# Kernel tuning notes

Hardware: AMD Instinct MI355X
Metric: run time of the kernel (lower is better)

## Reference

```python
import jax, jax.numpy as jnp
import numpy as np

C = 256        # in_channels
HEADS = 8
HD = 64        # dim_heads
INNER = HEADS * HD   # 512
G = 32         # norm_groups
FF = 4 * INNER # 2048
EPS = 1e-5


def setup_inputs() -> dict:
    key = jax.random.key(0)
    ks = jax.random.split(key, 12)
    r = lambda k, shp: jax.random.normal(k, shp, jnp.float32) * 0.02
    return {
        "x": jax.random.normal(ks[0], (1, C, 16, 16, 16), jnp.float32),
        "gn_g": jnp.ones((C,), jnp.float32),
        "gn_b": jnp.zeros((C,), jnp.float32),
        "w_in": r(ks[1], (INNER, C)),   # Conv3d 1x1x1 as (out,in) matrix
        "b_in": jnp.zeros((INNER,), jnp.float32),
        "wq": r(ks[2], (INNER, INNER)),
        "wk": r(ks[3], (INNER, INNER)),
        "wv": r(ks[4], (INNER, INNER)),
        "ln1_g": jnp.ones((INNER,), jnp.float32),
        "ln1_b": jnp.zeros((INNER,), jnp.float32),
        "ff_w1": r(ks[5], (FF, INNER)),
        "ff_b1": jnp.zeros((FF,), jnp.float32),
        "ff_w2": r(ks[6], (INNER, FF)),
        "ff_b2": jnp.zeros((INNER,), jnp.float32),
        "ln2_g": jnp.ones((INNER,), jnp.float32),
        "ln2_b": jnp.zeros((INNER,), jnp.float32),
        "w_out": r(ks[7], (C, INNER)),  # Conv3d 1x1x1 back to C
        "b_out": jnp.zeros((C,), jnp.float32),
    }


def _group_norm(x, g, b):
    # x: (B,C,D,H,W), G groups, normalize over (C//G, D, H, W)
    B, Cc, D, H, W = x.shape
    xr = x.reshape(B, G, Cc // G, D, H, W)
    mu = jnp.mean(xr, axis=(2, 3, 4, 5), keepdims=True)
    var = jnp.var(xr, axis=(2, 3, 4, 5), keepdims=True)
    xr = (xr - mu) * jax.lax.rsqrt(var + EPS)
    xn = xr.reshape(B, Cc, D, H, W)
    return xn * g[None, :, None, None, None] + b[None, :, None, None, None]


def _layer_norm(x, g, b):
    mu = jnp.mean(x, axis=-1, keepdims=True)
    var = jnp.var(x, axis=-1, keepdims=True)
    return (x - mu) * jax.lax.rsqrt(var + EPS) * g + b


def reference(x, gn_g, gn_b, w_in, b_in, wq, wk, wv, ln1_g, ln1_b,
              ff_w1, ff_b1, ff_w2, ff_b2, ln2_g, ln2_b, w_out, b_out):
    B, Cc, D, H, W = x.shape
    x_in = x
    # GroupNorm + proj_in (1x1x1 conv == channel matmul)
    h = _group_norm(x, gn_g, gn_b)
    t = jnp.einsum('bcdhw,oc->bodhw', h, w_in) + b_in[None, :, None, None, None]
    N = D * H * W
    t = t.reshape(B, INNER, N).transpose(0, 2, 1)  # (B, N, INNER)

    # self-attention (manual einsum softmax einsum)
    q = (t @ wq.T).reshape(B, N, HEADS, HD)
    k = (t @ wk.T).reshape(B, N, HEADS, HD)
    v = (t @ wv.T).reshape(B, N, HEADS, HD)
    scale = HD ** (-0.5)
    scores = jnp.einsum('bihd,bjhd->bhij', q, k) * scale  # (B,H,N,N)
    attn = jax.nn.softmax(scores, axis=-1)
    o = jnp.einsum('bhij,bjhd->bihd', attn, v).reshape(B, N, INNER)
    # out_proj is Identity (q_dim == inner_dim), dropout=0
    t = _layer_norm(o + t, ln1_g, ln1_b)

    # FeedForward: Linear -> GELU (erf) -> Linear
    ff = jax.nn.gelu(t @ ff_w1.T + ff_b1, approximate=False) @ ff_w2.T + ff_b2
    t = _layer_norm(ff + t, ln2_g, ln2_b)

    # proj_out + residual
    y = t.transpose(0, 2, 1).reshape(B, INNER, D, H, W)
    out = jnp.einsum('bidhw,oi->bodhw', y, w_out) + b_out[None, :, None, None, None]
    return out + x_in
```

## Files before the change

### kernel.cpp

```cpp
#include <hip/hip_runtime.h>
#include <hip/hip_bf16.h>

typedef unsigned short u16;
typedef __attribute__((ext_vector_type(8))) short short8;
typedef __attribute__((ext_vector_type(4))) float floatx4;

#define LOG2E 1.44269504088896f
#define CEXP (0.125f * LOG2E)

static __device__ __forceinline__ u16 f2b(float f) {
  union { float f; unsigned u; } v; v.f = f;
  unsigned r = v.u + 0x7fffu + ((v.u >> 16) & 1u);
  return (u16)(r >> 16);
}
static __device__ __forceinline__ float b2f(u16 b) {
  union { float f; unsigned u; } v; v.u = ((unsigned)b) << 16;
  return v.f;
}
static __device__ __forceinline__ void async16(const u16* g, u16* l) {
  __builtin_amdgcn_global_load_lds(
      (const __attribute__((address_space(1))) unsigned int*)g,
      (__attribute__((address_space(3))) unsigned int*)l, 16, 0, 0);
}
static __device__ __forceinline__ float fexp2(float x) {
  return __builtin_amdgcn_exp2f(x);
}

__global__ __launch_bounds__(256) void f2b_all(
    const float* __restrict__ s0, const float* __restrict__ s1, const float* __restrict__ s2,
    const float* __restrict__ s3, const float* __restrict__ s4, const float* __restrict__ s5,
    const float* __restrict__ s6, const float* __restrict__ x,
    u16* __restrict__ d_win, u16* __restrict__ d_qkv, u16* __restrict__ d_f1,
    u16* __restrict__ d_f2, u16* __restrict__ d_wout, float2* __restrict__ cstats) {
  if (blockIdx.x >= 12288) {
    int c = blockIdx.x - 12288;
    const float4* p4 = (const float4*)(x + (size_t)c * 4096);
    float s = 0.f, ss = 0.f;
#pragma unroll
    for (int j = 0; j < 4; j++) {
      float4 v = p4[j * 256 + threadIdx.x];
      s += v.x + v.y + v.z + v.w;
      ss += v.x * v.x + v.y * v.y + v.z * v.z + v.w * v.w;
    }
    for (int m = 1; m < 64; m <<= 1) { s += __shfl_xor(s, m); ss += __shfl_xor(ss, m); }
    __shared__ float sb[8];
    int w = threadIdx.x >> 6;
    if ((threadIdx.x & 63) == 0) { sb[w * 2] = s; sb[w * 2 + 1] = ss; }
    __syncthreads();
    if (threadIdx.x == 0)
      cstats[c] = float2{sb[0] + sb[2] + sb[4] + sb[6], sb[1] + sb[3] + sb[5] + sb[7]};
    return;
  }
  int i = blockIdx.x * 256 + threadIdx.x;
  if (i < 131072) { d_win[i] = f2b(s0[i]); return; }
  i -= 131072;
  if (i < 262144) { d_qkv[i] = f2b(s1[i]); return; }
  i -= 262144;
  if (i < 262144) { d_qkv[262144 + i] = f2b(s2[i]); return; }
  i -= 262144;
  if (i < 262144) { d_qkv[524288 + i] = f2b(s3[i]); return; }
  i -= 262144;
  if (i < 1048576) { d_f1[i] = f2b(s4[i]); return; }
  i -= 1048576;
  if (i < 1048576) { d_f2[i] = f2b(s5[i]); return; }
  i -= 1048576;
  d_wout[i] = f2b(s6[i]);
}

__global__ __launch_bounds__(256) void gn_apply(const float* __restrict__ x, const float2* __restrict__ cstats,
                                                const float* __restrict__ gg, const float* __restrict__ gb,
                                                u16* __restrict__ hn) {
  int idx = blockIdx.x * 256 + threadIdx.x;
  int c = idx >> 12, n = idx & 4095;
  int g = c >> 3;
  float s = 0.f, ss = 0.f;
#pragma unroll
  for (int j = 0; j < 8; j++) {
    float2 p = cstats[g * 8 + j];
    s += p.x; ss += p.y;
  }
  float mu = s / 32768.f;
  float rs = rsqrtf(ss / 32768.f - mu * mu + 1e-5f);
  float v = (x[idx] - mu) * rs * gg[c] + gb[c];
  hn[(size_t)n * 256 + c] = f2b(v);
}

#define FLAG_BIAS 1
#define FLAG_GELU 2
#define FLAG_C32 4
#define FLAG_C16 8
#define FLAG_QKV 16
#define FLAG_FINAL 32

__global__ __launch_bounds__(256) void gemm_bt(
    const u16* __restrict__ A, const u16* __restrict__ B, const float* __restrict__ bias,
    float* __restrict__ C32, u16* __restrict__ C16, const float* __restrict__ resid,
    int M, int N, int K, int flags) {
  __shared__ u16 As[128 * 64];
  __shared__ u16 Bs[64 * 64];
  const int t = threadIdx.x;
  const int lane = t & 63;
  const int w = t >> 6;
  const int ln = lane & 15;
  const int quad = lane >> 4;
  const int m0 = blockIdx.x * 128;
  const int n0 = blockIdx.y * 64;
  const int wm = (w >> 1) * 64;
  const int wn = (w & 1) * 32;

  floatx4 acc[4][2];
#pragma unroll
  for (int i = 0; i < 4; i++)
#pragma unroll
    for (int j = 0; j < 2; j++) acc[i][j] = floatx4{0.f, 0.f, 0.f, 0.f};

  for (int k0 = 0; k0 < K; k0 += 64) {
    __syncthreads();
#pragma unroll
    for (int i = 0; i < 4; ++i) {
      int s = i * 256 + t;
      int row = s >> 3;
      int kb = (s & 7) ^ (row & 7);
      async16(A + (size_t)(m0 + row) * K + k0 + kb * 8, &As[(i * 256 + (t & ~63)) * 8]);
    }
#pragma unroll
    for (int i = 0; i < 2; ++i) {
      int s = i * 256 + t;
      int row = s >> 3;
      int kb = (s & 7) ^ (row & 7);
      async16(B + (size_t)(n0 + row) * K + k0 + kb * 8, &Bs[(i * 256 + (t & ~63)) * 8]);
    }
    __syncthreads();
#pragma unroll
    for (int ksi = 0; ksi < 2; ksi++) {
      short8 af[4], bfr[2];
      int kb = ksi * 4 + quad;
#pragma unroll
      for (int i = 0; i < 4; i++) {
        int m = wm + i * 16 + ln;
        af[i] = *(const short8*)&As[(m * 8 + (kb ^ (m & 7))) * 8];
      }
#pragma unroll
      for (int j = 0; j < 2; j++) {
        int n = wn + j * 16 + ln;
        bfr[j] = *(const short8*)&Bs[(n * 8 + (kb ^ (n & 7))) * 8];
      }
#pragma unroll
      for (int i = 0; i < 4; i++)
#pragma unroll
        for (int j = 0; j < 2; j++)
          acc[i][j] = __builtin_amdgcn_mfma_f32_16x16x32_bf16(af[i], bfr[j], acc[i][j], 0, 0, 0);
    }
  }

#pragma unroll
  for (int i = 0; i < 4; i++) {
#pragma unroll
    for (int j = 0; j < 2; j++) {
      int n = n0 + wn + j * 16 + ln;
      float bv = (flags & FLAG_BIAS) ? bias[n] : 0.f;
#pragma unroll
      for (int r = 0; r < 4; r++) {
        int m = m0 + wm + i * 16 + quad * 4 + r;
        float v = acc[i][j][r] + bv;
        if (flags & FLAG_C32) C32[(size_t)m * N + n] = v;
        if (flags & FLAG_C16) C16[(size_t)m * N + n] = f2b(v);
        if (flags & FLAG_FINAL)
          C32[(size_t)m * N + n] = v + bias[m] + resid[(size_t)m * N + n];
      }
    }
  }
}

__global__ __launch_bounds__(256) void gemm_big(
    const u16* __restrict__ A, const u16* __restrict__ B, const float* __restrict__ bias,
    float* __restrict__ C32, float* __restrict__ C32b,
    u16* __restrict__ C16, u16* __restrict__ C16b, u16* __restrict__ C16T,
    int M, int N, int K, int flags) {
  __shared__ u16 As[128 * 64];
  __shared__ u16 Bs[128 * 64];
  const int t = threadIdx.x;
  const int lane = t & 63;
  const int w = t >> 6;
  const int ln = lane & 15;
  const int quad = lane >> 4;
  const int m0 = blockIdx.x * 128;
  const int n0 = blockIdx.y * 128;
  const int wm = (w >> 1) * 64;
  const int wn = (w & 1) * 64;
  const int kper = K / gridDim.z;
  const int kbeg = blockIdx.z * kper;

  floatx4 acc[4][4];
#pragma unroll
  for (int i = 0; i < 4; i++)
#pragma unroll
    for (int j = 0; j < 4; j++) acc[i][j] = floatx4{0.f, 0.f, 0.f, 0.f};

  for (int k0 = kbeg; k0 < kbeg + kper; k0 += 64) {
    __syncthreads();
#pragma unroll
    for (int i = 0; i < 4; ++i) {
      int s = i * 256 + t;
      int row = s >> 3;
      int kb = (s & 7) ^ (row & 7);
      async16(A + (size_t)(m0 + row) * K + k0 + kb * 8, &As[(i * 256 + (t & ~63)) * 8]);
      async16(B + (size_t)(n0 + row) * K + k0 + kb * 8, &Bs[(i * 256 + (t & ~63)) * 8]);
    }
    __syncthreads();
#pragma unroll
    for (int ksi = 0; ksi < 2; ksi++) {
      short8 af[4], bfr[4];
      int kb = ksi * 4 + quad;
#pragma unroll
      for (int i = 0; i < 4; i++) {
        int m = wm + i * 16 + ln;
        af[i] = *(const short8*)&As[(m * 8 + (kb ^ (m & 7))) * 8];
        int n = wn + i * 16 + ln;
        bfr[i] = *(const short8*)&Bs[(n * 8 + (kb ^ (n & 7))) * 8];
      }
#pragma unroll
      for (int i = 0; i < 4; i++)
#pragma unroll
        for (int j = 0; j < 4; j++)
          acc[i][j] = __builtin_amdgcn_mfma_f32_16x16x32_bf16(af[i], bfr[j], acc[i][j], 0, 0, 0);
    }
  }

  float* Cz = blockIdx.z ? C32b : C32;
#pragma unroll
  for (int i = 0; i < 4; i++) {
#pragma unroll
    for (int j = 0; j < 4; j++) {
      int n = n0 + wn + j * 16 + ln;
      float bv = ((flags & FLAG_BIAS) && blockIdx.z == 0) ? bias[n] : 0.f;
#pragma unroll
      for (int r = 0; r < 4; r++) {
        int m = m0 + wm + i * 16 + quad * 4 + r;
        float v = acc[i][j][r] + bv;
        if (flags & FLAG_GELU) v = 0.5f * v * (1.f + erff(v * 0.70710678118f));
        if (flags & FLAG_C32) Cz[(size_t)m * N + n] = v;
        if (flags & FLAG_C16) C16[(size_t)m * N + n] = f2b(v);
        if (flags & FLAG_QKV) {
          if (n < 512) C16[(size_t)m * 512 + n] = f2b(v * CEXP);
          else if (n < 1024) C16b[(size_t)m * 512 + (n - 512)] = f2b(v);
          else C16T[(size_t)(n - 1024) * M + m] = f2b(v);
        }
      }
    }
  }
}

__global__ __launch_bounds__(256, 4) void attn_kernel(
    const u16* __restrict__ Q, const u16* __restrict__ Km, const u16* __restrict__ VT,
    u16* __restrict__ Opart, float* __restrict__ ML, int Nseq, int kvLen) {
  __shared__ u16 Ks[64 * 64];
  __shared__ u16 Vs[64 * 64];
  __shared__ u16 Ps[4 * 32 * 64];
  const int t = threadIdx.x;
  const int lane = t & 63;
  const int w = t >> 6;
  const int ln = lane & 15;
  const int quad = lane >> 4;
  const int h = blockIdx.y;
  const int q0 = blockIdx.x * 128;
  const int split = blockIdx.z;
  const int kvbase = split * kvLen;
  u16* Opw = Opart + (size_t)split * Nseq * 512;
  u16* Pw = &Ps[w * 32 * 64];

  short8 qf[2][2];
#pragma unroll
  for (int qt = 0; qt < 2; qt++)
#pragma unroll
    for (int ksi = 0; ksi < 2; ksi++)
      qf[qt][ksi] = *(const short8*)&Q[(size_t)(q0 + w * 32 + qt * 16 + ln) * 512 + h * 64 + ksi * 32 + quad * 8];

  floatx4 accO[2][4];
#pragma unroll
  for (int qt = 0; qt < 2; qt++)
#pragma unroll
    for (int td = 0; td < 4; td++) accO[qt][td] = floatx4{0.f, 0.f, 0.f, 0.f};
  float lsum[2] = {0.f, 0.f};

  for (int kv = 0; kv < kvLen; kv += 64) {
    const int kv0 = kvbase + kv;
    __syncthreads();
#pragma unroll
    for (int i = 0; i < 2; ++i) {
      int s = i * 256 + t;
      int row = s >> 3;
      int kb = (s & 7) ^ (row & 7);
      async16(Km + (size_t)(kv0 + row) * 512 + h * 64 + kb * 8, &Ks[(i * 256 + (t & ~63)) * 8]);
      async16(VT + (size_t)(h * 64 + row) * Nseq + kv0 + kb * 8, &Vs[(i * 256 + (t & ~63)) * 8]);
    }
    __syncthreads();

    floatx4 accS[2][4];
#pragma unroll
    for (int qt = 0; qt < 2; qt++)
#pragma unroll
      for (int tj = 0; tj < 4; tj++) accS[qt][tj] = floatx4{0.f, 0.f, 0.f, 0.f};
#pragma unroll
    for (int ksi = 0; ksi < 2; ksi++) {
      int kb = ksi * 4 + quad;
      short8 kf[4];
#pragma unroll
      for (int tj = 0; tj < 4; tj++) {
        int key = tj * 16 + ln;
        kf[tj] = *(const short8*)&Ks[(key * 8 + (kb ^ (key & 7))) * 8];
      }
#pragma unroll
      for (int qt = 0; qt < 2; qt++)
#pragma unroll
        for (int tj = 0; tj < 4; tj++)
          accS[qt][tj] = __builtin_amdgcn_mfma_f32_16x16x32_bf16(kf[tj], qf[qt][ksi], accS[qt][tj], 0, 0, 0);
    }

#pragma unroll
    for (int qt = 0; qt < 2; qt++) {
      int q8 = (qt * 16 + ln) * 8;
#pragma unroll
      for (int tj = 0; tj < 4; tj++) {
        float p0 = fexp2(accS[qt][tj][0]);
        float p1 = fexp2(accS[qt][tj][1]);
        float p2 = fexp2(accS[qt][tj][2]);
        float p3 = fexp2(accS[qt][tj][3]);
        lsum[qt] += (p0 + p1) + (p2 + p3);
        __hip_bfloat162 a01 = __float22bfloat162_rn(float2{p0, p1});
        __hip_bfloat162 a23 = __float22bfloat162_rn(float2{p2, p3});
        uint2 pk;
        pk.x = *(unsigned*)&a01;
        pk.y = *(unsigned*)&a23;
        int kbx = tj * 2 + (quad >> 1);
        *(uint2*)&Pw[(q8 + (kbx ^ (ln & 7))) * 8 + (quad & 1) * 4] = pk;
      }
    }

#pragma unroll
    for (int ksi = 0; ksi < 2; ksi++) {
      int kb = ksi * 4 + quad;
      short8 pf[2];
#pragma unroll
      for (int qt = 0; qt < 2; qt++)
        pf[qt] = *(const short8*)&Pw[((qt * 16 + ln) * 8 + (kb ^ (ln & 7))) * 8];
#pragma unroll
      for (int td = 0; td < 4; td++) {
        int d = td * 16 + ln;
        short8 vf = *(const short8*)&Vs[(d * 8 + (kb ^ (d & 7))) * 8];
#pragma unroll
        for (int qt = 0; qt < 2; qt++)
          accO[qt][td] = __builtin_amdgcn_mfma_f32_16x16x32_bf16(vf, pf[qt], accO[qt][td], 0, 0, 0);
      }
    }
  }

#pragma unroll
  for (int qt = 0; qt < 2; qt++) {
    lsum[qt] += __shfl_xor(lsum[qt], 16);
    lsum[qt] += __shfl_xor(lsum[qt], 32);
  }
#pragma unroll
  for (int qt = 0; qt < 2; qt++) {
    int q = q0 + w * 32 + qt * 16 + ln;
#pragma unroll
    for (int td = 0; td < 4; td++) {
      __hip_bfloat162 p01 = __float22bfloat162_rn(float2{accO[qt][td][0], accO[qt][td][1]});
      __hip_bfloat162 p23 = __float22bfloat162_rn(float2{accO[qt][td][2], accO[qt][td][3]});
      uint2 pk;
      pk.x = *(unsigned*)&p01;
      pk.y = *(unsigned*)&p23;
      *(uint2*)&Opw[(size_t)q * 512 + h * 64 + td * 16 + quad * 4] = pk;
    }
    if (quad == 0)
      ML[((size_t)split * 8 + h) * Nseq + q] = lsum[qt];
  }
}

__global__ __launch_bounds__(256) void ln_attn(
    const u16* __restrict__ Opart, const float* __restrict__ ML,
    const float* __restrict__ t32, const float* __restrict__ g, const float* __restrict__ be,
    u16* __restrict__ o16) {
  int row = blockIdx.x;
  int t = threadIdx.x;
  float v[2];
#pragma unroll
  for (int p = 0; p < 2; p++) {
    int c = t + p * 256;
    int h = c >> 6;
    float lt = 0.f, acc = 0.f;
#pragma unroll
    for (int s = 0; s < 4; s++) {
      lt += ML[((size_t)s * 8 + h) * 4096 + row];
      acc += b2f(Opart[(size_t)s * 4096 * 512 + (size_t)row * 512 + c]);
    }
    v[p] = acc / lt + t32[(size_t)row * 512 + c];
  }
  float s = v[0] + v[1], ss = v[0] * v[0] + v[1] * v[1];
  for (int m = 1; m < 64; m <<= 1) { s += __shfl_xor(s, m); ss += __shfl_xor(ss, m); }
  __shared__ float sb[8];
  int w = t >> 6;
  if ((t & 63) == 0) { sb[w * 2] = s; sb[w * 2 + 1] = ss; }
  __syncthreads();
  s = sb[0] + sb[2] + sb[4] + sb[6];
  ss = sb[1] + sb[3] + sb[5] + sb[7];
  float mu = s / 512.f;
  float var = ss / 512.f - mu * mu;
  float rs = rsqrtf(var + 1e-5f);
#pragma unroll
  for (int p = 0; p < 2; p++) {
    int c = t + p * 256;
    o16[(size_t)row * 512 + c] = f2b((v[p] - mu) * rs * g[c] + be[c]);
  }
}

__global__ __launch_bounds__(256) void ln3(
    const float* __restrict__ a, const float* __restrict__ b, const u16* __restrict__ c16,
    const float* __restrict__ g, const float* __restrict__ be, u16* __restrict__ o16) {
  int row = blockIdx.x;
  int t = threadIdx.x;
  size_t base = (size_t)row * 512;
  float v0 = a[base + t] + b[base + t] + b2f(c16[base + t]);
  float v1 = a[base + t + 256] + b[base + t + 256] + b2f(c16[base + t + 256]);
  float s = v0 + v1, ss = v0 * v0 + v1 * v1;
  for (int m = 1; m < 64; m <<= 1) { s += __shfl_xor(s, m); ss += __shfl_xor(ss, m); }
  __shared__ float sb[8];
  int w = t >> 6;
  if ((t & 63) == 0) { sb[w * 2] = s; sb[w * 2 + 1] = ss; }
  __syncthreads();
  s = sb[0] + sb[2] + sb[4] + sb[6];
  ss = sb[1] + sb[3] + sb[5] + sb[7];
  float mu = s / 512.f;
  float var = ss / 512.f - mu * mu;
  float rs = rsqrtf(var + 1e-5f);
  o16[base + t] = f2b((v0 - mu) * rs * g[t] + be[t]);
  o16[base + t + 256] = f2b((v1 - mu) * rs * g[t + 256] + be[t + 256]);
}

extern "C" void kernel_launch(void* const* d_in, const int* in_sizes, int n_in,
                              void* d_out, int out_size, void* d_ws, size_t ws_size,
                              hipStream_t stream) {
  const float* x = (const float*)d_in[0];
  const float* gn_g = (const float*)d_in[1];
  const float* gn_b = (const float*)d_in[2];
  const float* w_in = (const float*)d_in[3];
  const float* b_in = (const float*)d_in[4];
  const float* wq = (const float*)d_in[5];
  const float* wk = (const float*)d_in[6];
  const float* wv = (const float*)d_in[7];
  const float* ln1_g = (const float*)d_in[8];
  const float* ln1_b = (const float*)d_in[9];
  const float* ff_w1 = (const float*)d_in[10];
  const float* ff_b1 = (const float*)d_in[11];
  const float* ff_w2 = (const float*)d_in[12];
  const float* ff_b2 = (const float*)d_in[13];
  const float* ln2_g = (const float*)d_in[14];
  const float* ln2_b = (const float*)d_in[15];
  const float* w_out = (const float*)d_in[16];
  const float* b_out = (const float*)d_in[17];
  float* out = (float*)d_out;
  char* ws = (char*)d_ws;

  u16* w_in16 = (u16*)(ws + 0);
  u16* wqkv16 = (u16*)(ws + 262144);
  u16* fw116 = (u16*)(ws + 1835008);
  u16* fw216 = (u16*)(ws + 3932160);
  u16* wout16 = (u16*)(ws + 6029312);
  float* t32 = (float*)(ws + 6291456);
  u16* t16 = (u16*)(ws + 14680064);
  u16* u16b = (u16*)(ws + 14680064);
  u16* qb = (u16*)(ws + 18874368);
  u16* kb = (u16*)(ws + 23068672);
  u16* vt = (u16*)(ws + 27262976);
  u16* opart = (u16*)(ws + 31457280);
  u16* g16 = (u16*)(ws + 31457280);
  float* ml = (float*)(ws + 48234496);
  u16* hn = (u16*)(ws + 49283072);
  float2* cstats = (float2*)(ws + 51380224);
  float* z32a = (float*)(ws + 6291456);
  float* z32b = (float*)(ws + 18874368);
  u16* zb = (u16*)(ws + 27262976);

  f2b_all<<<12544, 256, 0, stream>>>(w_in, wq, wk, wv, ff_w1, ff_w2, w_out, x,
                                     w_in16, wqkv16, fw116, fw216, wout16, cstats);
  gn_apply<<<4096, 256, 0, stream>>>(x, cstats, gn_g, gn_b, hn);

  gemm_bt<<<dim3(32, 8), 256, 0, stream>>>(hn, w_in16, b_in, t32, t16, nullptr,
                                           4096, 512, 256, FLAG_BIAS | FLAG_C32 | FLAG_C16);
  gemm_big<<<dim3(32, 12), 256, 0, stream>>>(t16, wqkv16, nullptr, nullptr, nullptr, qb, kb, vt,
                                             4096, 1536, 512, FLAG_QKV);
  attn_kernel<<<dim3(32, 8, 4), 256, 0, stream>>>(qb, kb, vt, opart, ml, 4096, 1024);
  ln_attn<<<4096, 256, 0, stream>>>(opart, ml, t32, ln1_g, ln1_b, u16b);
  gemm_big<<<dim3(32, 16), 256, 0, stream>>>(u16b, fw116, ff_b1, nullptr, nullptr, g16, nullptr, nullptr,
                                             4096, 2048, 512, FLAG_BIAS | FLAG_GELU | FLAG_C16);
  gemm_big<<<dim3(32, 4, 2), 256, 0, stream>>>(g16, fw216, ff_b2, z32a, z32b, nullptr, nullptr, nullptr,
                                               4096, 512, 2048, FLAG_BIAS | FLAG_C32);
  ln3<<<4096, 256, 0, stream>>>(z32a, z32b, u16b, ln2_g, ln2_b, zb);
  gemm_bt<<<dim3(2, 64), 256, 0, stream>>>(wout16, zb, b_out, out, nullptr, x,
                                           256, 4096, 512, FLAG_FINAL);
}
```

Before: 264.4 us.

## Double-buffer attention KV tiles, shrink intermediates to bf16, retile QKV GEMM

After: 250.1 us. 1.06x faster.

```diff
diff --git a/kernel.cpp b/kernel.cpp
--- a/kernel.cpp
+++ b/kernel.cpp
@@ -87,10 +87,9 @@
 
 #define FLAG_BIAS 1
 #define FLAG_GELU 2
-#define FLAG_C32 4
 #define FLAG_C16 8
-#define FLAG_QKV 16
 #define FLAG_FINAL 32
+#define FLAG_CZ 64
 
 __global__ __launch_bounds__(256) void gemm_bt(
     const u16* __restrict__ A, const u16* __restrict__ B, const float* __restrict__ bias,
@@ -163,7 +162,6 @@
       for (int r = 0; r < 4; r++) {
         int m = m0 + wm + i * 16 + quad * 4 + r;
         float v = acc[i][j][r] + bv;
-        if (flags & FLAG_C32) C32[(size_t)m * N + n] = v;
         if (flags & FLAG_C16) C16[(size_t)m * N + n] = f2b(v);
         if (flags & FLAG_FINAL)
           C32[(size_t)m * N + n] = v + bias[m] + resid[(size_t)m * N + n];
@@ -174,9 +172,7 @@
 
 __global__ __launch_bounds__(256) void gemm_big(
     const u16* __restrict__ A, const u16* __restrict__ B, const float* __restrict__ bias,
-    float* __restrict__ C32, float* __restrict__ C32b,
-    u16* __restrict__ C16, u16* __restrict__ C16b, u16* __restrict__ C16T,
-    int M, int N, int K, int flags) {
+    u16* __restrict__ C16, int M, int N, int K, int flags) {
   __shared__ u16 As[128 * 64];
   __shared__ u16 Bs[128 * 64];
   const int t = threadIdx.x;
@@ -227,7 +223,7 @@
     }
   }
 
-  float* Cz = blockIdx.z ? C32b : C32;
+  u16* Cdst = (flags & FLAG_CZ) ? C16 + (size_t)blockIdx.z * M * N : C16;
 #pragma unroll
   for (int i = 0; i < 4; i++) {
 #pragma unroll
@@ -239,13 +235,85 @@
         int m = m0 + wm + i * 16 + quad * 4 + r;
         float v = acc[i][j][r] + bv;
         if (flags & FLAG_GELU) v = 0.5f * v * (1.f + erff(v * 0.70710678118f));
-        if (flags & FLAG_C32) Cz[(size_t)m * N + n] = v;
-        if (flags & FLAG_C16) C16[(size_t)m * N + n] = f2b(v);
-        if (flags & FLAG_QKV) {
-          if (n < 512) C16[(size_t)m * 512 + n] = f2b(v * CEXP);
-          else if (n < 1024) C16b[(size_t)m * 512 + (n - 512)] = f2b(v);
-          else C16T[(size_t)(n - 1024) * M + m] = f2b(v);
-        }
+        Cdst[(size_t)m * N + n] = f2b(v);
+      }
+    }
+  }
+}
+
+__global__ __launch_bounds__(256) void gemm_qkv(
+    const u16* __restrict__ A, const u16* __restrict__ B,
+    u16* __restrict__ Cq, u16* __restrict__ Ck, u16* __restrict__ CvT,
+    int M, int K) {
+  __shared__ u16 As[64 * 64];
+  __shared__ u16 Bs[128 * 64];
+  const int t = threadIdx.x;
+  const int lane = t & 63;
+  const int w = t >> 6;
+  const int ln = lane & 15;
+  const int quad = lane >> 4;
+  const int m0 = blockIdx.x * 64;
+  const int n0 = blockIdx.y * 128;
+  const int wm = (w >> 1) * 32;
+  const int wn = (w & 1) * 64;
+
+  floatx4 acc[2][4];
+#pragma unroll
+  for (int i = 0; i < 2; i++)
+#pragma unroll
+    for (int j = 0; j < 4; j++) acc[i][j] = floatx4{0.f, 0.f, 0.f, 0.f};
+
+  for (int k0 = 0; k0 < K; k0 += 64) {
+    __syncthreads();
+#pragma unroll
+    for (int i = 0; i < 2; ++i) {
+      int s = i * 256 + t;
+      int row = s >> 3;
+      int kb = (s & 7) ^ (row & 7);
+      async16(A + (size_t)(m0 + row) * K + k0 + kb * 8, &As[(i * 256 + (t & ~63)) * 8]);
+    }
+#pragma unroll
+    for (int i = 0; i < 4; ++i) {
+      int s = i * 256 + t;
+      int row = s >> 3;
+      int kb = (s & 7) ^ (row & 7);
+      async16(B + (size_t)(n0 + row) * K + k0 + kb * 8, &Bs[(i * 256 + (t & ~63)) * 8]);
+    }
+    __syncthreads();
+#pragma unroll
+    for (int ksi = 0; ksi < 2; ksi++) {
+      short8 af[2], bfr[4];
+      int kb = ksi * 4 + quad;
+#pragma unroll
+      for (int i = 0; i < 2; i++) {
+        int m = wm + i * 16 + ln;
+        af[i] = *(const short8*)&As[(m * 8 + (kb ^ (m & 7))) * 8];
+      }
+#pragma unroll
+      for (int j = 0; j < 4; j++) {
+        int n = wn + j * 16 + ln;
+        bfr[j] = *(const short8*)&Bs[(n * 8 + (kb ^ (n & 7))) * 8];
+      }
+#pragma unroll
+      for (int i = 0; i < 2; i++)
+#pragma unroll
+        for (int j = 0; j < 4; j++)
+          acc[i][j] = __builtin_amdgcn_mfma_f32_16x16x32_bf16(af[i], bfr[j], acc[i][j], 0, 0, 0);
+    }
+  }
+
+#pragma unroll
+  for (int i = 0; i < 2; i++) {
+#pragma unroll
+    for (int j = 0; j < 4; j++) {
+      int n = n0 + wn + j * 16 + ln;
+#pragma unroll
+      for (int r = 0; r < 4; r++) {
+        int m = m0 + wm + i * 16 + quad * 4 + r;
+        float v = acc[i][j][r];
+        if (n < 512) Cq[(size_t)m * 512 + n] = f2b(v * CEXP);
+        else if (n < 1024) Ck[(size_t)m * 512 + (n - 512)] = f2b(v);
+        else CvT[(size_t)(n - 1024) * M + m] = f2b(v);
       }
     }
   }
@@ -254,8 +322,8 @@
 __global__ __launch_bounds__(256, 4) void attn_kernel(
     const u16* __restrict__ Q, const u16* __restrict__ Km, const u16* __restrict__ VT,
     u16* __restrict__ Opart, float* __restrict__ ML, int Nseq, int kvLen) {
-  __shared__ u16 Ks[64 * 64];
-  __shared__ u16 Vs[64 * 64];
+  __shared__ u16 Ks[2][64 * 64];
+  __shared__ u16 Vs[2][64 * 64];
   __shared__ u16 Ps[4 * 32 * 64];
   const int t = threadIdx.x;
   const int lane = t & 63;
@@ -283,18 +351,32 @@
     for (int td = 0; td < 4; td++) accO[qt][td] = floatx4{0.f, 0.f, 0.f, 0.f};
   float lsum[2] = {0.f, 0.f};
 
-  for (int kv = 0; kv < kvLen; kv += 64) {
-    const int kv0 = kvbase + kv;
-    __syncthreads();
-#pragma unroll
-    for (int i = 0; i < 2; ++i) {
-      int s = i * 256 + t;
-      int row = s >> 3;
-      int kb = (s & 7) ^ (row & 7);
-      async16(Km + (size_t)(kv0 + row) * 512 + h * 64 + kb * 8, &Ks[(i * 256 + (t & ~63)) * 8]);
-      async16(VT + (size_t)(h * 64 + row) * Nseq + kv0 + kb * 8, &Vs[(i * 256 + (t & ~63)) * 8]);
-    }
-    __syncthreads();
+  const int ntiles = kvLen >> 6;
+#pragma unroll
+  for (int i = 0; i < 2; ++i) {
+    int s = i * 256 + t;
+    int row = s >> 3;
+    int kb = (s & 7) ^ (row & 7);
+    async16(Km + (size_t)(kvbase + row) * 512 + h * 64 + kb * 8, &Ks[0][(i * 256 + (t & ~63)) * 8]);
+    async16(VT + (size_t)(h * 64 + row) * Nseq + kvbase + kb * 8, &Vs[0][(i * 256 + (t & ~63)) * 8]);
+  }
+
+  for (int tile = 0; tile < ntiles; ++tile) {
+    const int p = tile & 1;
+    __syncthreads();
+    if (tile + 1 < ntiles) {
+      const int kv0 = kvbase + (tile + 1) * 64;
+#pragma unroll
+      for (int i = 0; i < 2; ++i) {
+        int s = i * 256 + t;
+        int row = s >> 3;
+        int kb = (s & 7) ^ (row & 7);
+        async16(Km + (size_t)(kv0 + row) * 512 + h * 64 + kb * 8, &Ks[p ^ 1][(i * 256 + (t & ~63)) * 8]);
+        async16(VT + (size_t)(h * 64 + row) * Nseq + kv0 + kb * 8, &Vs[p ^ 1][(i * 256 + (t & ~63)) * 8]);
+      }
+    }
+    const u16* Kc = Ks[p];
+    const u16* Vc = Vs[p];
 
     floatx4 accS[2][4];
 #pragma unroll
@@ -308,7 +390,7 @@
 #pragma unroll
       for (int tj = 0; tj < 4; tj++) {
         int key = tj * 16 + ln;
-        kf[tj] = *(const short8*)&Ks[(key * 8 + (kb ^ (key & 7))) * 8];
+        kf[tj] = *(const short8*)&Kc[(key * 8 + (kb ^ (key & 7))) * 8];
       }
 #pragma unroll
       for (int qt = 0; qt < 2; qt++)
@@ -347,7 +429,7 @@
 #pragma unroll
       for (int td = 0; td < 4; td++) {
         int d = td * 16 + ln;
-        short8 vf = *(const short8*)&Vs[(d * 8 + (kb ^ (d & 7))) * 8];
+        short8 vf = *(const short8*)&Vc[(d * 8 + (kb ^ (d & 7))) * 8];
 #pragma unroll
         for (int qt = 0; qt < 2; qt++)
           accO[qt][td] = __builtin_amdgcn_mfma_f32_16x16x32_bf16(vf, pf[qt], accO[qt][td], 0, 0, 0);
@@ -379,49 +461,27 @@
 
 __global__ __launch_bounds__(256) void ln_attn(
     const u16* __restrict__ Opart, const float* __restrict__ ML,
-    const float* __restrict__ t32, const float* __restrict__ g, const float* __restrict__ be,
+    const u16* __restrict__ t16, const float* __restrict__ g, const float* __restrict__ be,
     u16* __restrict__ o16) {
   int row = blockIdx.x;
   int t = threadIdx.x;
-  float v[2];
-#pragma unroll
-  for (int p = 0; p < 2; p++) {
-    int c = t + p * 256;
-    int h = c >> 6;
-    float lt = 0.f, acc = 0.f;
-#pragma unroll
-    for (int s = 0; s < 4; s++) {
-      lt += ML[((size_t)s * 8 + h) * 4096 + row];
-      acc += b2f(Opart[(size_t)s * 4096 * 512 + (size_t)row * 512 + c]);
-    }
-    v[p] = acc / lt + t32[(size_t)row * 512 + c];
-  }
-  float s = v[0] + v[1], ss = v[0] * v[0] + v[1] * v[1];
-  for (int m = 1; m < 64; m <<= 1) { s += __shfl_xor(s, m); ss += __shfl_xor(ss, m); }
-  __shared__ float sb[8];
-  int w = t >> 6;
-  if ((t & 63) == 0) { sb[w * 2] = s; sb[w * 2 + 1] = ss; }
-  __syncthreads();
-  s = sb[0] + sb[2] + sb[4] + sb[6];
-  ss = sb[1] + sb[3] + sb[5] + sb[7];
-  float mu = s / 512.f;
-  float var = ss / 512.f - mu * mu;
-  float rs = rsqrtf(var + 1e-5f);
-#pragma unroll
-  for (int p = 0; p < 2; p++) {
-    int c = t + p * 256;
-    o16[(size_t)row * 512 + c] = f2b((v[p] - mu) * rs * g[c] + be[c]);
-  }
-}
-
-__global__ __launch_bounds__(256) void ln3(
-    const float* __restrict__ a, const float* __restrict__ b, const u16* __restrict__ c16,
-    const float* __restrict__ g, const float* __restrict__ be, u16* __restrict__ o16) {
-  int row = blockIdx.x;
-  int t = threadIdx.x;
   size_t base = (size_t)row * 512;
-  float v0 = a[base + t] + b[base + t] + b2f(c16[base + t]);
-  float v1 = a[base + t + 256] + b[base + t + 256] + b2f(c16[base + t + 256]);
+  int c0 = 2 * t;
+  int h = c0 >> 6;
+  float lt = 0.f;
+#pragma unroll
+  for (int s = 0; s < 4; s++) lt += ML[((size_t)s * 8 + h) * 4096 + row];
+  float a0 = 0.f, a1 = 0.f;
+#pragma unroll
+  for (int s = 0; s < 4; s++) {
+    unsigned oo = *(const unsigned*)&Opart[(size_t)s * 4096 * 512 + base + c0];
+    a0 += b2f((u16)(oo & 0xffff));
+    a1 += b2f((u16)(oo >> 16));
+  }
+  unsigned tt = *(const unsigned*)&t16[base + c0];
+  float inv = 1.0f / lt;
+  float v0 = a0 * inv + b2f((u16)(tt & 0xffff));
+  float v1 = a1 * inv + b2f((u16)(tt >> 16));
   float s = v0 + v1, ss = v0 * v0 + v1 * v1;
   for (int m = 1; m < 64; m <<= 1) { s += __shfl_xor(s, m); ss += __shfl_xor(ss, m); }
   __shared__ float sb[8];
@@ -433,8 +493,45 @@
   float mu = s / 512.f;
   float var = ss / 512.f - mu * mu;
   float rs = rsqrtf(var + 1e-5f);
-  o16[base + t] = f2b((v0 - mu) * rs * g[t] + be[t]);
-  o16[base + t + 256] = f2b((v1 - mu) * rs * g[t + 256] + be[t + 256]);
+  float2 gv = *(const float2*)&g[c0];
+  float2 bv = *(const float2*)&be[c0];
+  u16 r0 = f2b((v0 - mu) * rs * gv.x + bv.x);
+  u16 r1 = f2b((v1 - mu) * rs * gv.y + bv.y);
+  *(unsigned*)&o16[base + c0] = ((unsigned)r1 << 16) | r0;
+}
+
+__global__ __launch_bounds__(256) void ln_ff(
+    const u16* __restrict__ zp, const u16* __restrict__ u,
+    const float* __restrict__ g, const float* __restrict__ be, u16* __restrict__ o16) {
+  int row = blockIdx.x;
+  int t = threadIdx.x;
+  size_t base = (size_t)row * 512;
+  int c0 = 2 * t;
+  unsigned uu = *(const unsigned*)&u[base + c0];
+  float v0 = b2f((u16)(uu & 0xffff));
+  float v1 = b2f((u16)(uu >> 16));
+#pragma unroll
+  for (int z = 0; z < 4; z++) {
+    unsigned zz = *(const unsigned*)&zp[(size_t)z * 4096 * 512 + base + c0];
+    v0 += b2f((u16)(zz & 0xffff));
+    v1 += b2f((u16)(zz >> 16));
+  }
+  float s = v0 + v1, ss = v0 * v0 + v1 * v1;
+  for (int m = 1; m < 64; m <<= 1) { s += __shfl_xor(s, m); ss += __shfl_xor(ss, m); }
+  __shared__ float sb[8];
+  int w = t >> 6;
+  if ((t & 63) == 0) { sb[w * 2] = s; sb[w * 2 + 1] = ss; }
+  __syncthreads();
+  s = sb[0] + sb[2] + sb[4] + sb[6];
+  ss = sb[1] + sb[3] + sb[5] + sb[7];
+  float mu = s / 512.f;
+  float var = ss / 512.f - mu * mu;
+  float rs = rsqrtf(var + 1e-5f);
+  float2 gv = *(const float2*)&g[c0];
+  float2 bv = *(const float2*)&be[c0];
+  u16 r0 = f2b((v0 - mu) * rs * gv.x + bv.x);
+  u16 r1 = f2b((v1 - mu) * rs * gv.y + bv.y);
+  *(unsigned*)&o16[base + c0] = ((unsigned)r1 << 16) | r0;
 }
 
 extern "C" void kernel_launch(void* const* d_in, const int* in_sizes, int n_in,
@@ -466,36 +563,33 @@
   u16* fw116 = (u16*)(ws + 1835008);
   u16* fw216 = (u16*)(ws + 3932160);
   u16* wout16 = (u16*)(ws + 6029312);
-  float* t32 = (float*)(ws + 6291456);
+  u16* u16b = (u16*)(ws + 6291456);
+  u16* zp = (u16*)(ws + 10485760);
   u16* t16 = (u16*)(ws + 14680064);
-  u16* u16b = (u16*)(ws + 14680064);
   u16* qb = (u16*)(ws + 18874368);
   u16* kb = (u16*)(ws + 23068672);
   u16* vt = (u16*)(ws + 27262976);
+  u16* zb = (u16*)(ws + 27262976);
   u16* opart = (u16*)(ws + 31457280);
   u16* g16 = (u16*)(ws + 31457280);
   float* ml = (float*)(ws + 48234496);
   u16* hn = (u16*)(ws + 49283072);
   float2* cstats = (float2*)(ws + 51380224);
-  float* z32a = (float*)(ws + 6291456);
-  float* z32b = (float*)(ws + 18874368);
-  u16* zb = (u16*)(ws + 27262976);
 
   f2b_all<<<12544, 256, 0, stream>>>(w_in, wq, wk, wv, ff_w1, ff_w2, w_out, x,
                                      w_in16, wqkv16, fw116, fw216, wout16, cstats);
   gn_apply<<<4096, 256, 0, stream>>>(x, cstats, gn_g, gn_b, hn);
 
-  gemm_bt<<<dim3(32, 8), 256, 0, stream>>>(hn, w_in16, b_in, t32, t16, nullptr,
-                                           4096, 512, 256, FLAG_BIAS | FLAG_C32 | FLAG_C16);
-  gemm_big<<<dim3(32, 12), 256, 0, stream>>>(t16, wqkv16, nullptr, nullptr, nullptr, qb, kb, vt,
-                                             4096, 1536, 512, FLAG_QKV);
+  gemm_bt<<<dim3(32, 8), 256, 0, stream>>>(hn, w_in16, b_in, nullptr, t16, nullptr,
+                                           4096, 512, 256, FLAG_BIAS | FLAG_C16);
+  gemm_qkv<<<dim3(64, 12), 256, 0, stream>>>(t16, wqkv16, qb, kb, vt, 4096, 512);
   attn_kernel<<<dim3(32, 8, 4), 256, 0, stream>>>(qb, kb, vt, opart, ml, 4096, 1024);
-  ln_attn<<<4096, 256, 0, stream>>>(opart, ml, t32, ln1_g, ln1_b, u16b);
-  gemm_big<<<dim3(32, 16), 256, 0, stream>>>(u16b, fw116, ff_b1, nullptr, nullptr, g16, nullptr, nullptr,
+  ln_attn<<<4096, 256, 0, stream>>>(opart, ml, t16, ln1_g, ln1_b, u16b);
+  gemm_big<<<dim3(32, 16), 256, 0, stream>>>(u16b, fw116, ff_b1, g16,
                                              4096, 2048, 512, FLAG_BIAS | FLAG_GELU | FLAG_C16);
-  gemm_big<<<dim3(32, 4, 2), 256, 0, stream>>>(g16, fw216, ff_b2, z32a, z32b, nullptr, nullptr, nullptr,
-                                               4096, 512, 2048, FLAG_BIAS | FLAG_C32);
-  ln3<<<4096, 256, 0, stream>>>(z32a, z32b, u16b, ln2_g, ln2_b, zb);
+  gemm_big<<<dim3(32, 4, 4), 256, 0, stream>>>(g16, fw216, ff_b2, zp,
+                                               4096, 512, 2048, FLAG_BIAS | FLAG_CZ);
+  ln_ff<<<4096, 256, 0, stream>>>(zp, u16b, ln2_g, ln2_b, zb);
   gemm_bt<<<dim3(2, 64), 256, 0, stream>>>(wout16, zb, b_out, out, nullptr, x,
                                            256, 4096, 512, FLAG_FINAL);
 }
```
